# Optimization experiments

Measured on AMD Instinct MI355X. Metric: run time of the kernel, lower is better.

Reference implementation:

```python
import jax, jax.numpy as jnp
import numpy as np

G, K = 1024, 16           # groups, agents per group
N, T, D = G * K, 32, 64   # total agents, timesteps, feature dim
LN_EPS = 1e-5


def setup_inputs() -> dict:
    key = jax.random.key(0)
    ks = jax.random.split(key, 6)
    x = jax.random.normal(ks[0], (N, T, D), dtype=jnp.float32)
    # one-hot group assignment [G, N]; agents grouped contiguously (matches repeat_interleave order)
    seg = jnp.repeat(jnp.arange(G), K)                      # [N]
    batch_traffic_id_map = jax.nn.one_hot(seg, G, dtype=jnp.float32).T  # [G, N]
    num_traffics = jnp.full((G,), K, dtype=jnp.int64) if jax.config.jax_enable_x64 else jnp.full((G,), K, dtype=jnp.int32)
    s = 1.0 / np.sqrt(D)
    fc1_w = jax.random.uniform(ks[1], (D, D), jnp.float32, -s, s)
    fc1_b = jax.random.uniform(ks[2], (D,), jnp.float32, -s, s)
    ln_w = jnp.ones((D,), jnp.float32)
    ln_b = jnp.zeros((D,), jnp.float32)
    fc2_w = jax.random.uniform(ks[3], (D, D), jnp.float32, -s, s)
    fc2_b = jax.random.uniform(ks[4], (D,), jnp.float32, -s, s)
    return {"x": x, "batch_traffic_id_map": batch_traffic_id_map,
            "num_traffics": num_traffics, "fc1_w": fc1_w, "fc1_b": fc1_b,
            "ln_w": ln_w, "ln_b": ln_b, "fc2_w": fc2_w, "fc2_b": fc2_b}


def _mlp(x, fc1_w, fc1_b, ln_w, ln_b, fc2_w, fc2_b):
    h = x @ fc1_w.T + fc1_b
    mu = jnp.mean(h, axis=-1, keepdims=True)
    var = jnp.mean((h - mu) ** 2, axis=-1, keepdims=True)
    h = (h - mu) * jax.lax.rsqrt(var + LN_EPS) * ln_w + ln_b
    h = jax.nn.relu(h)
    return h @ fc2_w.T + fc2_b


def reference(x, batch_traffic_id_map, num_traffics, fc1_w, fc1_b, ln_w, ln_b, fc2_w, fc2_b):
    h = _mlp(x, fc1_w, fc1_b, ln_w, ln_b, fc2_w, fc2_b)      # [N,T,D]
    # segment sum via dense one-hot matmul (same math as torch.matmul(map, x.transpose(0,1)))
    x2 = jnp.einsum('gn,tnd->tgd', batch_traffic_id_map, h.transpose(1, 0, 2))  # [T,G,D]
    counts = jnp.where(num_traffics == 0, 1, num_traffics).astype(x2.dtype)     # [G]
    x2 = x2 / counts[None, :, None]
    # broadcast group mean back to agents (repeat_interleave == gather by segment id)
    seg = jnp.argmax(batch_traffic_id_map, axis=0)            # [N]
    x2n = jnp.take(x2, seg, axis=1)                           # [T,N,D]
    return jnp.concatenate((x2n.transpose(1, 0, 2), h), axis=2)  # [N,T,2D]
```

## Files before the change

### kernel.cpp

```cpp
#include <hip/hip_runtime.h>


typedef __attribute__((ext_vector_type(8))) short bfrag_t;
typedef __attribute__((ext_vector_type(4))) float f4_t;

__device__ __forceinline__ unsigned pkbf(float a, float b) {
#if defined(__has_builtin)
#if __has_builtin(__builtin_amdgcn_cvt_pk_bf16_f32)
  auto r = __builtin_amdgcn_cvt_pk_bf16_f32(a, b);
  union { decltype(r) v; unsigned u; } c; c.v = r; return c.u;
#define PKBF_DONE 1
#endif
#endif
#ifndef PKBF_DONE
  union { float f; unsigned u; } va, vb;
  va.f = a; vb.f = b;
  unsigned ra = va.u + 0x7fffu + ((va.u >> 16) & 1u);
  unsigned rb = vb.u + 0x7fffu + ((vb.u >> 16) & 1u);
  return (ra >> 16) | (rb & 0xffff0000u);
#endif
}

__device__ __forceinline__ short f2bf1(float a) {
  return (short)(unsigned short)(pkbf(a, a) & 0xffffu);
}

__device__ __forceinline__ bfrag_t cvt8(f4_t lo, f4_t hi) {
  union { bfrag_t f; unsigned u[4]; } c;
  c.u[0] = pkbf(lo[0], lo[1]);
  c.u[1] = pkbf(lo[2], lo[3]);
  c.u[2] = pkbf(hi[0], hi[1]);
  c.u[3] = pkbf(hi[2], hi[3]);
  return c.f;
}

template <int CTRL>
__device__ __forceinline__ float dpp_add(float v) {
  union { float f; int i; } a, b;
  a.f = v;
  b.i = __builtin_amdgcn_update_dpp(0, a.i, CTRL, 0xf, 0xf, true);
  return v + b.f;
}
__device__ __forceinline__ float rowsum16(float v) {
  v = dpp_add<0x121>(v);
  v = dpp_add<0x122>(v);
  v = dpp_add<0x124>(v);
  v = dpp_add<0x128>(v);
  return v;
}

constexpr int T_ = 32;
constexpr int D_ = 64;
#define LN_EPS 1e-5f

__device__ __forceinline__ int hswz(int row, int col) {
  return row * 64 + (col ^ ((row & 7) << 3));
}

__global__ __launch_bounds__(256, 4) void sg_fused(
    const float* __restrict__ x,
    const int*   __restrict__ num_traffics,
    const float* __restrict__ w1, const float* __restrict__ b1,
    const float* __restrict__ lnw, const float* __restrict__ lnb,
    const float* __restrict__ w2, const float* __restrict__ b2,
    float* __restrict__ out)
{
  __shared__ short   lds_h[4][16 * 64];
  __shared__ bfrag_t wlds[2][2][4][64];

  const int tid  = threadIdx.x;
  const int wave = tid >> 6;
  const int lane = tid & 63;
  const int m    = lane & 15;
  const int quad = lane >> 4;

  const int g = blockIdx.x;

  #pragma unroll
  for (int j = 0; j < 4; ++j) {
    const int c   = wave * 4 + j;
    const int mat = c >> 3;
    const int kk  = (c >> 2) & 1;
    const int tau = c & 3;
    const float* w = mat ? w2 : w1;
    const float* p = w + (tau*16 + m)*D_ + kk*32 + quad*8;
    const f4_t* q = reinterpret_cast<const f4_t*>(p);
    wlds[mat][kk][tau][lane] = cvt8(q[0], q[1]);
  }

  float bias1[4], bias2[4], lw[4], lb[4];
  #pragma unroll
  for (int tau = 0; tau < 4; ++tau) {
    bias1[tau] = b1[tau*16 + m];
    bias2[tau] = b2[tau*16 + m];
    lw[tau]    = lnw[tau*16 + m];
    lb[tau]    = lnb[tau*16 + m];
  }
  int cnt = num_traffics[g];
  if (cnt == 0) cnt = 1;
  const float inv_cnt = 1.0f / (float)cnt;

  __syncthreads();

  short* myld = lds_h[wave];

  for (int it = 0; it < 8; ++it) {
    const int t = wave*8 + it;

    const float* xrow = x + ((size_t)(g*16 + m) * T_ + t) * D_;
    const f4_t* xq = reinterpret_cast<const f4_t*>(xrow + quad*8);
    f4_t x0 = __builtin_nontemporal_load(xq);
    f4_t x1 = __builtin_nontemporal_load(xq + 1);
    const f4_t* xq2 = reinterpret_cast<const f4_t*>(xrow + 32 + quad*8);
    f4_t x2 = __builtin_nontemporal_load(xq2);
    f4_t x3 = __builtin_nontemporal_load(xq2 + 1);
    bfrag_t af0 = cvt8(x0, x1);
    bfrag_t af1 = cvt8(x2, x3);

    f4_t acc[4];
    #pragma unroll
    for (int tau = 0; tau < 4; ++tau) {
      f4_t c = {0.f, 0.f, 0.f, 0.f};
      c = __builtin_amdgcn_mfma_f32_16x16x32_bf16(af0, wlds[0][0][tau][lane], c, 0, 0, 0);
      c = __builtin_amdgcn_mfma_f32_16x16x32_bf16(af1, wlds[0][1][tau][lane], c, 0, 0, 0);
      acc[tau] = c;
    }

    float s[4] = {0,0,0,0}, sq[4] = {0,0,0,0};
    #pragma unroll
    for (int tau = 0; tau < 4; ++tau)
      #pragma unroll
      for (int i = 0; i < 4; ++i) {
        float v = acc[tau][i] + bias1[tau];
        acc[tau][i] = v;
        s[i] += v; sq[i] += v * v;
      }
    #pragma unroll
    for (int i = 0; i < 4; ++i) {
      s[i]  = rowsum16(s[i]);
      sq[i] = rowsum16(sq[i]);
    }
    float mu[4], rs[4];
    #pragma unroll
    for (int i = 0; i < 4; ++i) {
      mu[i] = s[i] * (1.0f / 64.0f);
      float var = sq[i] * (1.0f / 64.0f) - mu[i]*mu[i];
      rs[i] = rsqrtf(var + LN_EPS);
    }

    #pragma unroll
    for (int tau = 0; tau < 4; ++tau)
      #pragma unroll
      for (int i = 0; i < 4; ++i) {
        float v = (acc[tau][i] - mu[i]) * rs[i] * lw[tau] + lb[tau];
        v = fmaxf(v, 0.0f);
        const int row = quad*4 + i;
        myld[hswz(row, tau*16 + m)] = f2bf1(v);
      }

    const int sw = (m & 7) << 3;
    bfrag_t hf0 = *reinterpret_cast<const bfrag_t*>(&myld[m*64 + ((0*32 + quad*8) ^ sw)]);
    bfrag_t hf1 = *reinterpret_cast<const bfrag_t*>(&myld[m*64 + ((1*32 + quad*8) ^ sw)]);

    f4_t acc2[4];
    #pragma unroll
    for (int tau = 0; tau < 4; ++tau) {
      f4_t c = {0.f, 0.f, 0.f, 0.f};
      c = __builtin_amdgcn_mfma_f32_16x16x32_bf16(hf0, wlds[1][0][tau][lane], c, 0, 0, 0);
      c = __builtin_amdgcn_mfma_f32_16x16x32_bf16(hf1, wlds[1][1][tau][lane], c, 0, 0, 0);
      acc2[tau] = c;
    }

    float csum[4];
    #pragma unroll
    for (int tau = 0; tau < 4; ++tau) {
      float t0 = 0.f;
      #pragma unroll
      for (int i = 0; i < 4; ++i) {
        float v = acc2[tau][i] + bias2[tau];
        acc2[tau][i] = v;
        t0 += v;
      }
      csum[tau] = t0;
    }
    #pragma unroll
    for (int mask = 16; mask < 64; mask <<= 1)
      #pragma unroll
      for (int tau = 0; tau < 4; ++tau)
        csum[tau] += __shfl_xor(csum[tau], mask, 64);
    float mean[4];
    #pragma unroll
    for (int tau = 0; tau < 4; ++tau) mean[tau] = csum[tau] * inv_cnt;

    #pragma unroll
    for (int i = 0; i < 4; ++i) {
      const size_t base = ((size_t)(g*16 + quad*4 + i) * T_ + t) * (2*D_);
      #pragma unroll
      for (int tau = 0; tau < 4; ++tau) {
        __builtin_nontemporal_store(mean[tau],    out + base + tau*16 + m);
        __builtin_nontemporal_store(acc2[tau][i], out + base + 64 + tau*16 + m);
      }
    }
  }
}

extern "C" void kernel_launch(void* const* d_in, const int* in_sizes, int n_in,
                              void* d_out, int out_size, void* d_ws, size_t ws_size,
                              hipStream_t stream) {
  const float* x   = (const float*)d_in[0];
  const int*   ntr = (const int*)d_in[2];
  const float* w1  = (const float*)d_in[3];
  const float* b1  = (const float*)d_in[4];
  const float* lnw = (const float*)d_in[5];
  const float* lnb = (const float*)d_in[6];
  const float* w2  = (const float*)d_in[7];
  const float* b2  = (const float*)d_in[8];
  float* out = (float*)d_out;

  dim3 grid(1024), block(256);
  hipLaunchKernelGGL(sg_fused, grid, block, 0, stream,
                     x, ntr, w1, b1, lnw, lnb, w2, b2, out);
}
```

Baseline: 427.3 us.

## Prefetch x tiles asynchronously into LDS one timestep ahead

Replaces the per-iteration direct global loads of x with global_load_lds transfers into a per-wave LDS buffer. The tile for the next timestep is issued right after the current one is read into registers, so its latency overlaps the MFMA, LayerNorm and store work. Rows use an XOR swizzle to avoid LDS bank conflicts. Progress relies on hand-written s_waitcnt counts (vmcnt(32) assumes the 32 stores per iteration retire in order with the loads), adds 16 KB of LDS per block, and uses a single buffer that is reused each step.

```diff
diff --git a/kernel.cpp b/kernel.cpp
--- a/kernel.cpp
+++ b/kernel.cpp
@@ -57,6 +57,12 @@
   return row * 64 + (col ^ ((row & 7) << 3));
 }
 
+typedef const __attribute__((address_space(1))) unsigned int* gp1_t;
+typedef __attribute__((address_space(3))) unsigned int* lp3_t;
+__device__ __forceinline__ void load16_lds(const void* g, void* l) {
+  __builtin_amdgcn_global_load_lds((gp1_t)g, (lp3_t)l, 16, 0, 0);
+}
+
 __global__ __launch_bounds__(256, 4) void sg_fused(
     const float* __restrict__ x,
     const int*   __restrict__ num_traffics,
@@ -67,6 +73,7 @@
 {
   __shared__ short   lds_h[4][16 * 64];
   __shared__ bfrag_t wlds[2][2][4][64];
+  __shared__ float   lds_x[4][1024];
 
   const int tid  = threadIdx.x;
   const int wave = tid >> 6;
@@ -75,6 +82,27 @@
   const int quad = lane >> 4;
 
   const int g = blockIdx.x;
+
+  float* xl = lds_x[wave];
+
+  const int lrow = lane >> 4;
+  const int gsl  = (lane >> 1) & 7;
+  const int half = lane & 1;
+  const char* xb = (const char*)x;
+#define XSRC(j) (xb + (size_t)((g*16 + (4*(j) + lrow)) * T_ + wave*8) * 256 \
+                    + (size_t)(((gsl ^ ((4*(j) + lrow) & 7)) * 32) + half*16))
+  const char* p0 = XSRC(0);
+  const char* p1 = XSRC(1);
+  const char* p2 = XSRC(2);
+  const char* p3 = XSRC(3);
+#undef XSRC
+
+  load16_lds(p0, &xl[0]);
+  load16_lds(p1, &xl[256]);
+  load16_lds(p2, &xl[512]);
+  load16_lds(p3, &xl[768]);
+  __builtin_amdgcn_sched_barrier(0);
+  p0 += 256; p1 += 256; p2 += 256; p3 += 256;
 
   #pragma unroll
   for (int j = 0; j < 4; ++j) {
@@ -104,18 +132,31 @@
 
   short* myld = lds_h[wave];
 
+  const int s0 = quad ^ (m & 7);
+  const int s1 = s0 ^ 4;
+
   for (int it = 0; it < 8; ++it) {
     const int t = wave*8 + it;
 
-    const float* xrow = x + ((size_t)(g*16 + m) * T_ + t) * D_;
-    const f4_t* xq = reinterpret_cast<const f4_t*>(xrow + quad*8);
-    f4_t x0 = __builtin_nontemporal_load(xq);
-    f4_t x1 = __builtin_nontemporal_load(xq + 1);
-    const f4_t* xq2 = reinterpret_cast<const f4_t*>(xrow + 32 + quad*8);
-    f4_t x2 = __builtin_nontemporal_load(xq2);
-    f4_t x3 = __builtin_nontemporal_load(xq2 + 1);
+    asm volatile("s_waitcnt vmcnt(32)" ::: "memory");
+
+    const f4_t* xa = reinterpret_cast<const f4_t*>(&xl[m*64 + s0*8]);
+    f4_t x0 = xa[0], x1 = xa[1];
+    const f4_t* xc = reinterpret_cast<const f4_t*>(&xl[m*64 + s1*8]);
+    f4_t x2 = xc[0], x3 = xc[1];
     bfrag_t af0 = cvt8(x0, x1);
     bfrag_t af1 = cvt8(x2, x3);
+
+    if (it < 7) {
+      asm volatile("s_waitcnt lgkmcnt(0)" ::: "memory");
+      __builtin_amdgcn_sched_barrier(0);
+      load16_lds(p0, &xl[0]);
+      load16_lds(p1, &xl[256]);
+      load16_lds(p2, &xl[512]);
+      load16_lds(p3, &xl[768]);
+      __builtin_amdgcn_sched_barrier(0);
+      p0 += 256; p1 += 256; p2 += 256; p3 += 256;
+    }
 
     f4_t acc[4];
     #pragma unroll
```

Result: faster. 410.0 us (-4.0%).
